# Performance work log

Measured on AMD Instinct MI355X. Metric: run time of the kernel, lower is better.

The kernel has to match this reference:

```python
import jax, jax.numpy as jnp
import numpy as np
from jax import lax

D_MODEL = 1024
D_STATE = 16
D_CONV = 4
EXPAND = 2
D_INNER = D_MODEL * EXPAND          # 2048
DT_RANK = (D_MODEL + 15) // 16      # 64
B, L = 2, 1024


def setup_inputs() -> dict:
    key = jax.random.key(0)
    ks = jax.random.split(key, 11)
    s = lambda d: 1.0 / np.sqrt(d)
    x = jax.random.normal(ks[0], (B, L, D_MODEL), jnp.float32)
    W_in = jax.random.normal(ks[1], (D_MODEL, 2 * D_INNER), jnp.float32) * s(D_MODEL)
    conv_w = jax.random.normal(ks[2], (D_INNER, D_CONV), jnp.float32) * s(D_CONV)
    conv_b = jax.random.normal(ks[3], (D_INNER,), jnp.float32) * 0.01
    W_x = jax.random.normal(ks[4], (D_INNER, DT_RANK + 2 * D_STATE), jnp.float32) * s(D_INNER)
    W_dt = jax.random.normal(ks[5], (DT_RANK, D_INNER), jnp.float32) * s(DT_RANK)
    # dt bias init as in the torch module: inverse-softplus of dt in [1e-3, 1e-1]
    dt = jnp.exp(jax.random.uniform(ks[6], (D_INNER,), jnp.float32)
                 * (np.log(0.1) - np.log(0.001)) + np.log(0.001))
    dt = jnp.clip(dt, 1e-4, None)
    b_dt = dt + jnp.log(-jnp.expm1(-dt))
    W_out = jax.random.normal(ks[7], (D_INNER, D_MODEL), jnp.float32) * s(D_INNER)
    a = jnp.arange(1, D_STATE + 1, dtype=jnp.float32)[None, :].repeat(D_INNER, axis=0)
    a = a + jax.random.uniform(ks[8], (D_INNER, D_STATE), jnp.float32) * 0.1
    A_log = jnp.log(a)
    D_param = jnp.ones((D_INNER,), jnp.float32)
    return {"x": x, "W_in": W_in, "conv_w": conv_w, "conv_b": conv_b,
            "W_x": W_x, "W_dt": W_dt, "b_dt": b_dt, "W_out": W_out,
            "A_log": A_log, "D_param": D_param}


def _mamba_forward(x, W_in, conv_w, conv_b, W_x, W_dt, b_dt, W_out, A_log, D_param):
    # input projection -> two branches
    xz = x @ W_in                                  # [B,L,2*Di]
    xb, zb = jnp.split(xz, 2, axis=-1)             # each [B,L,Di]
    # causal depthwise conv1d (kernel D_CONV, left pad)
    xp = jnp.pad(xb, ((0, 0), (D_CONV - 1, 0), (0, 0)))
    seq = xb.shape[1]
    xc = conv_b + sum(xp[:, j:j + seq, :] * conv_w[:, j] for j in range(D_CONV))
    u = jax.nn.silu(xc)                            # [B,L,Di]
    # data-dependent SSM parameters
    params = u @ W_x                               # [B,L,dt_rank+2*Ds]
    dlt, b_term, c_term = jnp.split(params, [DT_RANK, DT_RANK + D_STATE], axis=-1)
    delta = jax.nn.softplus(dlt @ W_dt + b_dt)     # [B,L,Di]
    a = -jnp.exp(A_log)                            # [Di,Ds]
    delta_a = jnp.exp(delta[..., None] * a)        # [B,L,Di,Ds]
    delta_b_u = (delta * u)[..., None] * b_term[:, :, None, :]  # [B,L,Di,Ds]

    def step(state, inp):
        da_t, dbu_t, c_t = inp                     # [B,Di,Ds],[B,Di,Ds],[B,Ds]
        state = da_t * state + dbu_t
        y_t = jnp.einsum('bdn,bn->bd', state, c_t)
        return state, y_t

    init = jnp.zeros((x.shape[0], D_INNER, D_STATE), jnp.float32)
    xs = (delta_a.transpose(1, 0, 2, 3),
          delta_b_u.transpose(1, 0, 2, 3),
          c_term.transpose(1, 0, 2))
    _, ys = lax.scan(step, init, xs)               # ys: [L,B,Di]
    y = ys.transpose(1, 0, 2) + D_param * u        # skip term D*u
    y = y * jax.nn.silu(zb)
    return y @ W_out                               # [B,L,Dm]


def reference(x, W_in, conv_w, conv_b, W_x, W_dt, b_dt, W_out, A_log, D_param):
    return _mamba_forward(x, W_in, conv_w, conv_b, W_x, W_dt, b_dt, W_out, A_log, D_param)
```

## Files before the change

kernel.cpp:

```cpp
#include <hip/hip_runtime.h>
#include <hip/hip_bf16.h>
#include <math.h>

#define DM 1024
#define DI 2048
#define DS 16
#define DTR 64
#define NB 2
#define LL 1024
#define MM (NB*LL)
#define NC 32
#define CL (LL/NC)
#define XSPLIT 8
#define XKC (DI/XSPLIT)

typedef unsigned short u16;
typedef __bf16 bf16x8 __attribute__((ext_vector_type(8)));
typedef float f32x4 __attribute__((ext_vector_type(4)));
typedef const __attribute__((address_space(1))) void gas_void;
typedef __attribute__((address_space(3))) void las_void;

__device__ __forceinline__ float sigmoidf_(float x){ return 1.f/(1.f+__expf(-x)); }
__device__ __forceinline__ float siluf_(float x){ return x*sigmoidf_(x); }
__device__ __forceinline__ float softplusf_(float x){ return fmaxf(x,0.f)+__logf(1.f+__expf(-fabsf(x))); }
__device__ __forceinline__ u16 f2b(float f){
  __hip_bfloat16 h = __float2bfloat16(f);
  return __builtin_bit_cast(unsigned short, h);
}
__device__ __forceinline__ size_t smap(size_t i){ return ((i>>11)<<12) + (i&2047); }
__device__ __forceinline__ void gld16(const u16* g, u16* l){
  __builtin_amdgcn_global_load_lds(
      reinterpret_cast<gas_void*>((unsigned long long)g),
      reinterpret_cast<las_void*>((unsigned)(unsigned long long)l), 16, 0, 0);
}

__global__ __launch_bounds__(512) void gemm_mfma_kern(
    const u16* __restrict__ A, const u16* __restrict__ Bt,
    float* __restrict__ C, int M, int N, int lda, int KS, int TN, int TM)
{
  __shared__ __attribute__((aligned(16))) u16 As[128*32];
  __shared__ __attribute__((aligned(16))) u16 Bs[128*32];
  const unsigned t = threadIdx.x;
  const unsigned l = t & 63;
  const unsigned w = t >> 6;
  const unsigned wm = w >> 2, wn = w & 3;
  const int q8  = (int)gridDim.x >> 3;
  const int id2 = ((int)blockIdx.x & 7) * q8 + ((int)blockIdx.x >> 3);
  const int zz  = id2 / (TN*TM);
  const int rr  = id2 % (TN*TM);
  const int bm  = (rr / TN) * 128;
  const int bn  = (rr % TN) * 128;
  const int kbeg = zz * KS;
  const unsigned srow = t >> 2;
  const unsigned scol = (t & 3) * 8;
  f32x4 acc[4][2] = {};
  for (int k0 = kbeg; k0 < kbeg + KS; k0 += 32) {
    gld16(A  + (size_t)(bm + srow)*lda + k0 + scol, As + t*8);
    gld16(Bt + (size_t)(bn + srow)*lda + k0 + scol, Bs + t*8);
    __syncthreads();
    bf16x8 af[4], bfr[2];
    #pragma unroll
    for (int m = 0; m < 4; ++m)
      af[m] = *(const bf16x8*)(As + (wm*64 + m*16 + (l & 15))*32 + (l >> 4)*8);
    #pragma unroll
    for (int n = 0; n < 2; ++n)
      bfr[n] = *(const bf16x8*)(Bs + (wn*32 + n*16 + (l & 15))*32 + (l >> 4)*8);
    #pragma unroll
    for (int m = 0; m < 4; ++m)
      #pragma unroll
      for (int n = 0; n < 2; ++n)
        acc[m][n] = __builtin_amdgcn_mfma_f32_16x16x32_bf16(af[m], bfr[n], acc[m][n], 0, 0, 0);
    __syncthreads();
  }
  float* Cz = C + (size_t)zz*M*N;
  #pragma unroll
  for (int m = 0; m < 4; ++m) {
    #pragma unroll
    for (int n = 0; n < 2; ++n) {
      const int col = bn + wn*32 + n*16 + (l & 15);
      #pragma unroll
      for (int q = 0; q < 4; ++q) {
        const int row = bm + wm*64 + m*16 + (l >> 4)*4 + q;
        Cz[(size_t)row*N + col] = acc[m][n][q];
      }
    }
  }
}

__global__ __launch_bounds__(256) void reduce4_kern(
    const float* __restrict__ part, float* __restrict__ out)
{
  const size_t i = ((size_t)blockIdx.x*256 + threadIdx.x) * 4;
  float4 s = *(const float4*)(part + i);
  #pragma unroll
  for (int ks = 1; ks < 4; ++ks) {
    const float4 v = *(const float4*)(part + (size_t)ks*MM*DM + i);
    s.x+=v.x; s.y+=v.y; s.z+=v.z; s.w+=v.w;
  }
  *(float4*)(out + i) = s;
}

__global__ __launch_bounds__(256) void dtproj_kern(
    const float* __restrict__ params, const float* __restrict__ W_dt,
    const float* __restrict__ b_dt, float* __restrict__ delta)
{
  __shared__ __align__(16) float Ad[32][DTR];
  __shared__ __align__(16) float Wd[DTR][128];
  const int tid = threadIdx.x;
  const int m0 = (blockIdx.x >> 4) * 32;
  const int c0 = (blockIdx.x & 15) * 128;
  #pragma unroll
  for (int i = 0; i < 2; ++i) {
    const int fq = i*256 + tid;
    const int r = fq >> 4, q = fq & 15;
    *(float4*)&Ad[r][q*4] = *(const float4*)(params + (size_t)(m0+r)*96 + q*4);
  }
  #pragma unroll
  for (int i = 0; i < 8; ++i) {
    const int fq = i*256 + tid;
    const int r = fq >> 5, q = fq & 31;
    *(float4*)&Wd[r][q*4] = *(const float4*)(W_dt + (size_t)r*DI + c0 + q*4);
  }
  __syncthreads();
  const int tr = tid >> 5;
  const int tc = tid & 31;
  f32x4 acc[4] = {};
  #pragma unroll
  for (int k0 = 0; k0 < DTR; k0 += 4) {
    float4 a[4], wv[4];
    #pragma unroll
    for (int i = 0; i < 4; ++i) a[i] = *(const float4*)&Ad[tr*4+i][k0];
    #pragma unroll
    for (int j = 0; j < 4; ++j) wv[j] = *(const float4*)&Wd[k0+j][tc*4];
    #pragma unroll
    for (int i = 0; i < 4; ++i) {
      const float ai[4] = {a[i].x, a[i].y, a[i].z, a[i].w};
      #pragma unroll
      for (int j = 0; j < 4; ++j) {
        acc[i][0] = fmaf(ai[j], wv[j].x, acc[i][0]);
        acc[i][1] = fmaf(ai[j], wv[j].y, acc[i][1]);
        acc[i][2] = fmaf(ai[j], wv[j].z, acc[i][2]);
        acc[i][3] = fmaf(ai[j], wv[j].w, acc[i][3]);
      }
    }
  }
  const float4 b4 = *(const float4*)(b_dt + c0 + tc*4);
  #pragma unroll
  for (int i = 0; i < 4; ++i) {
    float4 o;
    o.x = softplusf_(acc[i][0] + b4.x);
    o.y = softplusf_(acc[i][1] + b4.y);
    o.z = softplusf_(acc[i][2] + b4.z);
    o.w = softplusf_(acc[i][3] + b4.w);
    *(float4*)(delta + (size_t)(m0 + tr*4 + i)*DI + c0 + tc*4) = o;
  }
}

__global__ __launch_bounds__(256) void transpose_cvt_kern(
    const float* __restrict__ in, u16* __restrict__ out, int R, int C)
{
  __shared__ float tile[32][33];
  const int r0 = blockIdx.y*32, c0 = blockIdx.x*32;
  const int tr = threadIdx.x >> 3, tc4 = (threadIdx.x & 7) * 4;
  float4 v = *(const float4*)(in + (size_t)(r0+tr)*C + c0 + tc4);
  tile[tr][tc4+0] = v.x; tile[tr][tc4+1] = v.y;
  tile[tr][tc4+2] = v.z; tile[tr][tc4+3] = v.w;
  __syncthreads();
  ushort4 o;
  o.x = f2b(tile[tc4+0][tr]);
  o.y = f2b(tile[tc4+1][tr]);
  o.z = f2b(tile[tc4+2][tr]);
  o.w = f2b(tile[tc4+3][tr]);
  *(ushort4*)(out + (size_t)(c0+tr)*R + r0 + tc4) = o;
}

__global__ __launch_bounds__(256) void cvt_bf16_kern(
    const float* __restrict__ in, int ld, int C, u16* __restrict__ out, int rows)
{
  const int i = blockIdx.x*256 + threadIdx.x;
  if (i >= rows*(C/4)) return;
  const int row = i / (C/4);
  const int cq  = (i % (C/4)) * 4;
  float4 v = *(const float4*)(in + (size_t)row*ld + cq);
  ushort4 o; o.x=f2b(v.x); o.y=f2b(v.y); o.z=f2b(v.z); o.w=f2b(v.w);
  *(ushort4*)(out + (size_t)row*C + cq) = o;
}

__global__ __launch_bounds__(256) void xproj_part_kern(
    const float* __restrict__ u, const float* __restrict__ W_x,
    float* __restrict__ part)
{
  __shared__ __align__(16) float Uk[XKC][32];
  const int tid = threadIdx.x;
  const int m0 = (blockIdx.x & 63) * 32;
  const int ks = blockIdx.x >> 6;
  const int k0 = ks * XKC;
  #pragma unroll
  for (int i = 0; i < 8; ++i) {
    const int fq = i*256 + tid;
    const int r = fq & 31, kq = fq >> 5;
    const float4 v = *(const float4*)(u + (size_t)(m0+r)*DI + k0 + kq*4);
    Uk[kq*4+0][r] = v.x; Uk[kq*4+1][r] = v.y;
    Uk[kq*4+2][r] = v.z; Uk[kq*4+3][r] = v.w;
  }
  __syncthreads();
  const int r4 = tid >> 5;
  const int c  = tid & 31;
  f32x4 a0 = {}, a1 = {}, a2 = {};
  #pragma unroll 4
  for (int k = 0; k < XKC; ++k) {
    const float* w = W_x + (size_t)(k0+k)*96 + c;
    const float w0 = w[0], w1 = w[32], w2 = w[64];
    const float4 uv = *(const float4*)&Uk[k][r4*4];
    const float ur[4] = {uv.x, uv.y, uv.z, uv.w};
    #pragma unroll
    for (int i = 0; i < 4; ++i) {
      a0[i] = fmaf(ur[i], w0, a0[i]);
      a1[i] = fmaf(ur[i], w1, a1[i]);
      a2[i] = fmaf(ur[i], w2, a2[i]);
    }
  }
  #pragma unroll
  for (int i = 0; i < 4; ++i) {
    float* p = part + ((size_t)ks*MM + m0 + r4*4 + i)*96 + c;
    p[0] = a0[i]; p[32] = a1[i]; p[64] = a2[i];
  }
}

__global__ __launch_bounds__(256) void xproj_reduce_kern(
    const float* __restrict__ part, float* __restrict__ params)
{
  const int i = blockIdx.x*256 + threadIdx.x;
  float4 s = {0.f,0.f,0.f,0.f};
  #pragma unroll
  for (int ks = 0; ks < XSPLIT; ++ks) {
    float4 v = *(const float4*)(part + (size_t)ks*MM*96 + (size_t)i*4);
    s.x+=v.x; s.y+=v.y; s.z+=v.z; s.w+=v.w;
  }
  *(float4*)(params + (size_t)i*4) = s;
}

__global__ __launch_bounds__(256) void conv_silu_kern(
    const float* __restrict__ xz, const float* __restrict__ conv_w,
    const float* __restrict__ conv_b, float* __restrict__ u)
{
  const int idx = blockIdx.x * 256 + threadIdx.x;
  const int d4 = (idx & (DI/4 - 1)) * 4;
  const int ml = idx >> 9;
  const int l  = ml & (LL-1);
  const int base = ml - l;
  const float4 w0 = *(const float4*)(conv_w + (d4+0)*4);
  const float4 w1 = *(const float4*)(conv_w + (d4+1)*4);
  const float4 w2 = *(const float4*)(conv_w + (d4+2)*4);
  const float4 w3 = *(const float4*)(conv_w + (d4+3)*4);
  const float wt[4][4] = {{w0.x,w0.y,w0.z,w0.w},{w1.x,w1.y,w1.z,w1.w},
                          {w2.x,w2.y,w2.z,w2.w},{w3.x,w3.y,w3.z,w3.w}};
  float4 acc = *(const float4*)(conv_b + d4);
  #pragma unroll
  for (int j = 0; j < 4; ++j) {
    const int ls = l - 3 + j;
    if (ls >= 0) {
      const float4 v = *(const float4*)(xz + (size_t)(base + ls)*(2*DI) + d4);
      acc.x = fmaf(v.x, wt[0][j], acc.x);
      acc.y = fmaf(v.y, wt[1][j], acc.y);
      acc.z = fmaf(v.z, wt[2][j], acc.z);
      acc.w = fmaf(v.w, wt[3][j], acc.w);
    }
  }
  float4 o;
  o.x = siluf_(acc.x); o.y = siluf_(acc.y);
  o.z = siluf_(acc.z); o.w = siluf_(acc.w);
  *(float4*)(u + (size_t)idx*4) = o;
}

__global__ __launch_bounds__(256) void scan_local_kern(
    const float* __restrict__ delta, const float* __restrict__ u,
    const float* __restrict__ params, const float* __restrict__ A_log,
    float* __restrict__ Pc, float* __restrict__ Fc)
{
  const int flat = blockIdx.x*256 + threadIdx.x;
  const int q  = flat & 3;
  const int ch = flat >> 2;
  const int d  = ch & (DI-1);
  const int c  = (ch >> 11) & (NC-1);
  const int b  = ch >> 16;
  const float4 al = *(const float4*)(A_log + d*DS + q*4);
  const float a0=-expf(al.x), a1=-expf(al.y), a2=-expf(al.z), a3=-expf(al.w);
  const size_t lbase = (size_t)b*LL + (size_t)c*CL;
  const float* dl = delta + lbase*DI + d;
  const float* uu = u     + lbase*DI + d;
  const float* pr = params + lbase*96 + DTR + q*4;
  float s0=0.f,s1=0.f,s2=0.f,s3=0.f, dtsum=0.f;
  #pragma unroll 4
  for (int l = 0; l < CL; ++l) {
    const float dt = dl[(size_t)l*DI];
    const float ut = uu[(size_t)l*DI];
    const float4 B4 = *(const float4*)(pr + l*96);
    const float dtu = dt*ut;
    s0 = fmaf(__expf(dt*a0), s0, dtu*B4.x);
    s1 = fmaf(__expf(dt*a1), s1, dtu*B4.y);
    s2 = fmaf(__expf(dt*a2), s2, dtu*B4.z);
    s3 = fmaf(__expf(dt*a3), s3, dtu*B4.w);
    dtsum += dt;
  }
  const size_t base = (((size_t)(b*DI + d))*NC + c)*DS + q*4;
  float4 P4; P4.x=__expf(dtsum*a0); P4.y=__expf(dtsum*a1);
  P4.z=__expf(dtsum*a2); P4.w=__expf(dtsum*a3);
  *(float4*)(Pc + smap(base)) = P4;
  *(float4*)(Fc + smap(base)) = make_float4(s0,s1,s2,s3);
}

__global__ __launch_bounds__(256) void scan_combine_kern(
    float* __restrict__ PS, const float* __restrict__ Fc)
{
  const int idx = blockIdx.x*256 + threadIdx.x;
  const size_t base = (size_t)(idx >> 4) * (NC*DS) + (idx & 15);
  float s = 0.f;
  #pragma unroll
  for (int c = 0; c < NC; ++c) {
    const size_t a = smap(base + c*DS);
    const float P = PS[a], F = Fc[a];
    PS[a] = s;
    s = fmaf(P, s, F);
  }
}

__global__ __launch_bounds__(256) void scan_apply_kern(
    const float* __restrict__ delta, const float* __restrict__ u,
    const float* __restrict__ params, const float* __restrict__ xz,
    const float* __restrict__ A_log, const float* __restrict__ D_param,
    const float* __restrict__ Sinit, u16* __restrict__ y16)
{
  const int flat = blockIdx.x*256 + threadIdx.x;
  const int q  = flat & 3;
  const int ch = flat >> 2;
  const int d  = ch & (DI-1);
  const int c  = (ch >> 11) & (NC-1);
  const int b  = ch >> 16;
  const float4 al = *(const float4*)(A_log + d*DS + q*4);
  const float a0=-expf(al.x), a1=-expf(al.y), a2=-expf(al.z), a3=-expf(al.w);
  const float Dp = D_param[d];
  const size_t lbase = (size_t)b*LL + (size_t)c*CL;
  const float* dl = delta + lbase*DI + d;
  const float* uu = u     + lbase*DI + d;
  const float* pb = params + lbase*96 + DTR + q*4;
  const float* pc = params + lbase*96 + DTR + DS + q*4;
  const float* zp = xz + lbase*(2*DI) + DI + d;
  u16* yo = y16 + lbase*DI + d;
  const size_t base = (((size_t)(b*DI + d))*NC + c)*DS + q*4;
  const float4 s4 = *(const float4*)(Sinit + smap(base));
  float s0=s4.x, s1=s4.y, s2=s4.z, s3=s4.w;
  #pragma unroll 4
  for (int l = 0; l < CL; ++l) {
    const float dt = dl[(size_t)l*DI];
    const float ut = uu[(size_t)l*DI];
    const float4 B4 = *(const float4*)(pb + l*96);
    const float4 C4 = *(const float4*)(pc + l*96);
    const float dtu = dt*ut;
    s0 = fmaf(__expf(dt*a0), s0, dtu*B4.x);
    s1 = fmaf(__expf(dt*a1), s1, dtu*B4.y);
    s2 = fmaf(__expf(dt*a2), s2, dtu*B4.z);
    s3 = fmaf(__expf(dt*a3), s3, dtu*B4.w);
    float part = s0*C4.x + s1*C4.y + s2*C4.z + s3*C4.w;
    part += __shfl_xor(part, 1);
    part += __shfl_xor(part, 2);
    if (q == 0) {
      const float z = zp[(size_t)l*(2*DI)];
      yo[(size_t)l*DI] = f2b((part + Dp*ut) * siluf_(z));
    }
  }
}

extern "C" void kernel_launch(void* const* d_in, const int* in_sizes, int n_in,
                              void* d_out, int out_size, void* d_ws, size_t ws_size,
                              hipStream_t stream)
{
  const float* x      = (const float*)d_in[0];
  const float* W_in   = (const float*)d_in[1];
  const float* conv_w = (const float*)d_in[2];
  const float* conv_b = (const float*)d_in[3];
  const float* W_x    = (const float*)d_in[4];
  const float* W_dt   = (const float*)d_in[5];
  const float* b_dt   = (const float*)d_in[6];
  const float* W_out  = (const float*)d_in[7];
  const float* A_log  = (const float*)d_in[8];
  const float* D_par  = (const float*)d_in[9];
  float* out = (float*)d_out;

  float* xz     = (float*)d_ws;
  float* u      = xz + (size_t)MM*2*DI;
  float* params = u  + (size_t)MM*DI;
  float* delta  = params + (size_t)MM*96;
  u16*  pool    = (u16*)(delta + (size_t)MM*DI);
  u16* xb16 = pool;
  u16* Wi_t = (u16*)out;
  u16* Wo_t   = pool;
  u16* yb16   = pool + (size_t)DM*DI;
  float* xpart = out;
  float* Pc = xz;
  float* Fc = xz + (size_t)1024*4096;
  float* g4part = xz;

  dim3 blk(256);
  dim3 blk512(512);
  cvt_bf16_kern<<<(MM*DM/4 + 255)/256, blk, 0, stream>>>(x, DM, DM, xb16, MM);
  transpose_cvt_kern<<<dim3(2*DI/32, DM/32), blk, 0, stream>>>(W_in, Wi_t, DM, 2*DI);
  gemm_mfma_kern<<<512, blk512, 0, stream>>>(xb16, Wi_t, xz, MM, 2*DI, DM, DM, 32, 16);
  conv_silu_kern<<<(MM*DI/4)/256, blk, 0, stream>>>(xz, conv_w, conv_b, u);
  xproj_part_kern<<<64*XSPLIT, blk, 0, stream>>>(u, W_x, xpart);
  xproj_reduce_kern<<<(MM*96/4)/256, blk, 0, stream>>>(xpart, params);
  dtproj_kern<<<1024, blk, 0, stream>>>(params, W_dt, b_dt, delta);
  scan_local_kern<<<(NB*NC*DI*4)/256, blk, 0, stream>>>(delta, u, params, A_log, Pc, Fc);
  scan_combine_kern<<<(NB*DI*DS)/256, blk, 0, stream>>>(Pc, Fc);
  scan_apply_kern<<<(NB*NC*DI*4)/256, blk, 0, stream>>>(delta, u, params, xz, A_log, D_par, Pc, yb16);
  transpose_cvt_kern<<<dim3(DM/32, DI/32), blk, 0, stream>>>(W_out, Wo_t, DI, DM);
  gemm_mfma_kern<<<512, blk512, 0, stream>>>(yb16, Wo_t, g4part, MM, DM, DI, DI/4, 8, 16);
  reduce4_kern<<<(MM*DM/4)/256, blk, 0, stream>>>(g4part, out);
}
```

Before: 186.6 us.

## Give each scan thread all 16 states and stage B/C in shared memory

Each scan_local and scan_apply thread now owns one (batch, chunk, channel) with all 16 state elements in registers, where before four threads each held four states. The per-chunk B and C vectors are loaded once per block into LDS, and the cross-lane shuffle reduction in the apply kernel is removed. This cuts redundant loads of delta, u and z by four and removes the shuffles. In exchange there are four times fewer threads (128 blocks' worth of parallelism), higher register pressure, and a longer serial dependency chain per thread, which may hurt latency hiding.

Measured after the change: 188.8 us. About the same (+1.2%).

```diff
diff --git a/kernel.cpp b/kernel.cpp
--- a/kernel.cpp
+++ b/kernel.cpp
@@ -278,36 +278,56 @@
     const float* __restrict__ params, const float* __restrict__ A_log,
     float* __restrict__ Pc, float* __restrict__ Fc)
 {
+  __shared__ __align__(16) float Bs[CL][DS];
   const int flat = blockIdx.x*256 + threadIdx.x;
-  const int q  = flat & 3;
-  const int ch = flat >> 2;
-  const int d  = ch & (DI-1);
-  const int c  = (ch >> 11) & (NC-1);
-  const int b  = ch >> 16;
-  const float4 al = *(const float4*)(A_log + d*DS + q*4);
-  const float a0=-expf(al.x), a1=-expf(al.y), a2=-expf(al.z), a3=-expf(al.w);
+  const int d = flat & (DI-1);
+  const int c = (flat >> 11) & (NC-1);
+  const int b = flat >> 16;
   const size_t lbase = (size_t)b*LL + (size_t)c*CL;
+  if (threadIdx.x < CL*DS/4) {
+    const int row = threadIdx.x >> 2, col4 = (threadIdx.x & 3)*4;
+    *(float4*)&Bs[row][col4] = *(const float4*)(params + (lbase+row)*96 + DTR + col4);
+  }
+  __syncthreads();
+  float a[DS];
+  #pragma unroll
+  for (int i = 0; i < 4; ++i) {
+    const float4 al = *(const float4*)(A_log + d*DS + i*4);
+    a[i*4+0] = -expf(al.x); a[i*4+1] = -expf(al.y);
+    a[i*4+2] = -expf(al.z); a[i*4+3] = -expf(al.w);
+  }
   const float* dl = delta + lbase*DI + d;
   const float* uu = u     + lbase*DI + d;
-  const float* pr = params + lbase*96 + DTR + q*4;
-  float s0=0.f,s1=0.f,s2=0.f,s3=0.f, dtsum=0.f;
-  #pragma unroll 4
+  float s[DS];
+  #pragma unroll
+  for (int n = 0; n < DS; ++n) s[n] = 0.f;
+  float dtsum = 0.f;
+  #pragma unroll 2
   for (int l = 0; l < CL; ++l) {
     const float dt = dl[(size_t)l*DI];
     const float ut = uu[(size_t)l*DI];
-    const float4 B4 = *(const float4*)(pr + l*96);
     const float dtu = dt*ut;
-    s0 = fmaf(__expf(dt*a0), s0, dtu*B4.x);
-    s1 = fmaf(__expf(dt*a1), s1, dtu*B4.y);
-    s2 = fmaf(__expf(dt*a2), s2, dtu*B4.z);
-    s3 = fmaf(__expf(dt*a3), s3, dtu*B4.w);
     dtsum += dt;
-  }
-  const size_t base = (((size_t)(b*DI + d))*NC + c)*DS + q*4;
-  float4 P4; P4.x=__expf(dtsum*a0); P4.y=__expf(dtsum*a1);
-  P4.z=__expf(dtsum*a2); P4.w=__expf(dtsum*a3);
-  *(float4*)(Pc + smap(base)) = P4;
-  *(float4*)(Fc + smap(base)) = make_float4(s0,s1,s2,s3);
+    const float4 B0 = *(const float4*)&Bs[l][0];
+    const float4 B1 = *(const float4*)&Bs[l][4];
+    const float4 B2 = *(const float4*)&Bs[l][8];
+    const float4 B3 = *(const float4*)&Bs[l][12];
+    const float Bv[DS] = {B0.x,B0.y,B0.z,B0.w, B1.x,B1.y,B1.z,B1.w,
+                          B2.x,B2.y,B2.z,B2.w, B3.x,B3.y,B3.z,B3.w};
+    #pragma unroll
+    for (int n = 0; n < DS; ++n)
+      s[n] = fmaf(__expf(dt*a[n]), s[n], dtu*Bv[n]);
+  }
+  const size_t base = (((size_t)(b*DI + d))*NC + c)*DS;
+  #pragma unroll
+  for (int i = 0; i < 4; ++i) {
+    float4 P4, F4;
+    P4.x = __expf(dtsum*a[i*4+0]); P4.y = __expf(dtsum*a[i*4+1]);
+    P4.z = __expf(dtsum*a[i*4+2]); P4.w = __expf(dtsum*a[i*4+3]);
+    F4.x = s[i*4+0]; F4.y = s[i*4+1]; F4.z = s[i*4+2]; F4.w = s[i*4+3];
+    *(float4*)(Pc + smap(base + i*4)) = P4;
+    *(float4*)(Fc + smap(base + i*4)) = F4;
+  }
 }
 
 __global__ __launch_bounds__(256) void scan_combine_kern(
@@ -331,43 +351,66 @@
     const float* __restrict__ A_log, const float* __restrict__ D_param,
     const float* __restrict__ Sinit, u16* __restrict__ y16)
 {
+  __shared__ __align__(16) float Bs[CL][DS];
+  __shared__ __align__(16) float Cs[CL][DS];
   const int flat = blockIdx.x*256 + threadIdx.x;
-  const int q  = flat & 3;
-  const int ch = flat >> 2;
-  const int d  = ch & (DI-1);
-  const int c  = (ch >> 11) & (NC-1);
-  const int b  = ch >> 16;
-  const float4 al = *(const float4*)(A_log + d*DS + q*4);
-  const float a0=-expf(al.x), a1=-expf(al.y), a2=-expf(al.z), a3=-expf(al.w);
+  const int d = flat & (DI-1);
+  const int c = (flat >> 11) & (NC-1);
+  const int b = flat >> 16;
+  const size_t lbase = (size_t)b*LL + (size_t)c*CL;
+  {
+    const int t = threadIdx.x;
+    const int row = (t & 127) >> 2, col4 = (t & 3)*4;
+    if (t < 128)
+      *(float4*)&Bs[row][col4] = *(const float4*)(params + (lbase+row)*96 + DTR + col4);
+    else
+      *(float4*)&Cs[row][col4] = *(const float4*)(params + (lbase+row)*96 + DTR + DS + col4);
+  }
+  __syncthreads();
+  float a[DS];
+  #pragma unroll
+  for (int i = 0; i < 4; ++i) {
+    const float4 al = *(const float4*)(A_log + d*DS + i*4);
+    a[i*4+0] = -expf(al.x); a[i*4+1] = -expf(al.y);
+    a[i*4+2] = -expf(al.z); a[i*4+3] = -expf(al.w);
+  }
   const float Dp = D_param[d];
-  const size_t lbase = (size_t)b*LL + (size_t)c*CL;
   const float* dl = delta + lbase*DI + d;
   const float* uu = u     + lbase*DI + d;
-  const float* pb = params + lbase*96 + DTR + q*4;
-  const float* pc = params + lbase*96 + DTR + DS + q*4;
   const float* zp = xz + lbase*(2*DI) + DI + d;
   u16* yo = y16 + lbase*DI + d;
-  const size_t base = (((size_t)(b*DI + d))*NC + c)*DS + q*4;
-  const float4 s4 = *(const float4*)(Sinit + smap(base));
-  float s0=s4.x, s1=s4.y, s2=s4.z, s3=s4.w;
-  #pragma unroll 4
+  const size_t base = (((size_t)(b*DI + d))*NC + c)*DS;
+  float s[DS];
+  #pragma unroll
+  for (int i = 0; i < 4; ++i) {
+    const float4 s4 = *(const float4*)(Sinit + smap(base + i*4));
+    s[i*4+0]=s4.x; s[i*4+1]=s4.y; s[i*4+2]=s4.z; s[i*4+3]=s4.w;
+  }
+  #pragma unroll 2
   for (int l = 0; l < CL; ++l) {
     const float dt = dl[(size_t)l*DI];
     const float ut = uu[(size_t)l*DI];
-    const float4 B4 = *(const float4*)(pb + l*96);
-    const float4 C4 = *(const float4*)(pc + l*96);
+    const float z  = zp[(size_t)l*(2*DI)];
     const float dtu = dt*ut;
-    s0 = fmaf(__expf(dt*a0), s0, dtu*B4.x);
-    s1 = fmaf(__expf(dt*a1), s1, dtu*B4.y);
-    s2 = fmaf(__expf(dt*a2), s2, dtu*B4.z);
-    s3 = fmaf(__expf(dt*a3), s3, dtu*B4.w);
-    float part = s0*C4.x + s1*C4.y + s2*C4.z + s3*C4.w;
-    part += __shfl_xor(part, 1);
-    part += __shfl_xor(part, 2);
-    if (q == 0) {
-      const float z = zp[(size_t)l*(2*DI)];
-      yo[(size_t)l*DI] = f2b((part + Dp*ut) * siluf_(z));
+    const float4 B0 = *(const float4*)&Bs[l][0];
+    const float4 B1 = *(const float4*)&Bs[l][4];
+    const float4 B2 = *(const float4*)&Bs[l][8];
+    const float4 B3 = *(const float4*)&Bs[l][12];
+    const float4 C0 = *(const float4*)&Cs[l][0];
+    const float4 C1 = *(const float4*)&Cs[l][4];
+    const float4 C2 = *(const float4*)&Cs[l][8];
+    const float4 C3 = *(const float4*)&Cs[l][12];
+    const float Bv[DS] = {B0.x,B0.y,B0.z,B0.w, B1.x,B1.y,B1.z,B1.w,
+                          B2.x,B2.y,B2.z,B2.w, B3.x,B3.y,B3.z,B3.w};
+    const float Cv[DS] = {C0.x,C0.y,C0.z,C0.w, C1.x,C1.y,C1.z,C1.w,
+                          C2.x,C2.y,C2.z,C2.w, C3.x,C3.y,C3.z,C3.w};
+    float part = 0.f;
+    #pragma unroll
+    for (int n = 0; n < DS; ++n) {
+      s[n] = fmaf(__expf(dt*a[n]), s[n], dtu*Bv[n]);
+      part = fmaf(s[n], Cv[n], part);
     }
+    yo[(size_t)l*DI] = f2b((part + Dp*ut) * siluf_(z));
   }
 }
 
@@ -410,9 +453,9 @@
   xproj_part_kern<<<64*XSPLIT, blk, 0, stream>>>(u, W_x, xpart);
   xproj_reduce_kern<<<(MM*96/4)/256, blk, 0, stream>>>(xpart, params);
   dtproj_kern<<<1024, blk, 0, stream>>>(params, W_dt, b_dt, delta);
-  scan_local_kern<<<(NB*NC*DI*4)/256, blk, 0, stream>>>(delta, u, params, A_log, Pc, Fc);
+  scan_local_kern<<<(NB*NC*DI)/256, blk, 0, stream>>>(delta, u, params, A_log, Pc, Fc);
   scan_combine_kern<<<(NB*DI*DS)/256, blk, 0, stream>>>(Pc, Fc);
-  scan_apply_kern<<<(NB*NC*DI*4)/256, blk, 0, stream>>>(delta, u, params, xz, A_log, D_par, Pc, yb16);
+  scan_apply_kern<<<(NB*NC*DI)/256, blk, 0, stream>>>(delta, u, params, xz, A_log, D_par, Pc, yb16);
   transpose_cvt_kern<<<dim3(DM/32, DI/32), blk, 0, stream>>>(W_out, Wo_t, DI, DM);
   gemm_mfma_kern<<<512, blk512, 0, stream>>>(yb16, Wo_t, g4part, MM, DM, DI, DI/4, 8, 16);
   reduce4_kern<<<(MM*DM/4)/256, blk, 0, stream>>>(g4part, out);
```
